# Kernel tuning notes

Measured on AMD Instinct MI355X. Metric: run time of the kernel, lower is better.

Reference implementation:

```python
import jax, jax.numpy as jnp
import numpy as np

SPACE_SIZE = 224
PATCH_SIZE = 16
PATCH_NUM = 196
GRID = SPACE_SIZE // PATCH_SIZE          # 14 patches per axis
OFFSET = 1.0 / (2.0 * GRID)              # half patch width in canonical coords
N_POINTS = 4_000_000


def _pipeline(pc_np):
    """Host-side index pipeline, mirroring the torch module's np.unique usage.
    All outputs are constants w.r.t. differentiation (pure integer indexing)."""
    # voxel quantization: canonical [0,1) -> [0,224); truncation matches torch .long()
    vox = (pc_np * SPACE_SIZE).astype(np.int64)                      # [N,3]
    unq, _, inv = np.unique(vox, return_index=True, return_inverse=True, axis=0)
    inv = inv.reshape(-1)
    num_voxels = unq.shape[0]
    patch = unq // PATCH_SIZE                                        # [U,3]
    # patch_select: keep PATCH_NUM random occupied patches
    p_unq, p_inv = np.unique(patch, return_inverse=True, axis=0)
    p_inv = p_inv.reshape(-1)
    P = p_unq.shape[0]
    sel = np.zeros(P, dtype=bool)
    sel[:PATCH_NUM] = True
    sel = sel[np.random.default_rng(0).permutation(P)]               # randperm mask
    sel_idx = np.nonzero(sel[p_inv])[0]                              # [M] sorted == bool-mask gather
    unq_sel = unq[sel_idx]
    patch_sel = patch[sel_idx]
    patch_unq, patch_unq_indx, patch_unq_inv = np.unique(
        patch_sel, return_index=True, return_inverse=True, axis=0)
    return dict(inv=inv, num_voxels=int(num_voxels), sel_idx=sel_idx,
                unq_sel=unq_sel, patch_sel=patch_sel,
                patch_unq_indx=patch_unq_indx,
                patch_unq_inv=patch_unq_inv.reshape(-1),
                cur_length=int(patch_unq.shape[0]))


def setup_inputs() -> dict:
    key = jax.random.key(0)
    pc_np = np.asarray(jax.random.uniform(key, (N_POINTS, 3), dtype=jnp.float32))
    idx = _pipeline(pc_np)
    return {
        "pc": jnp.asarray(pc_np),
        "inv": jnp.asarray(idx["inv"]),
        "sel_idx": jnp.asarray(idx["sel_idx"]),
        "unq_sel": jnp.asarray(idx["unq_sel"]),
        "patch_sel": jnp.asarray(idx["patch_sel"]),
        "patch_unq_indx": jnp.asarray(idx["patch_unq_indx"]),
        "patch_unq_inv": jnp.asarray(idx["patch_unq_inv"]),
        "num_voxels": idx["num_voxels"],
        "cur_length": idx["cur_length"],
    }


def reference(pc, inv, sel_idx, unq_sel, patch_sel, patch_unq_indx,
              patch_unq_inv, num_voxels, cur_length):
    # scatter-max pooling of point coords into occupied voxels, then select voxels
    features = jax.ops.segment_max(pc, inv, num_segments=num_voxels)[sel_idx]  # [M,3]
    M = features.shape[0]
    # absolute patch coords: patch_indx * 2*offset
    coords_abs = patch_sel.astype(pc.dtype) * (2.0 * OFFSET)                   # [M,3]
    # in-voxel relative hash (x + y*16 + z*256)
    cr = unq_sel % PATCH_SIZE
    coords_rela_query = cr[:, 0] + cr[:, 1] * PATCH_SIZE + cr[:, 2] * PATCH_SIZE ** 2
    # per-patch mean of voxel coords (scatter-mean), gathered back per voxel
    seg_sum = jax.ops.segment_sum(features, patch_unq_inv, num_segments=cur_length)
    seg_cnt = jax.ops.segment_sum(jnp.ones((M, 1), pc.dtype), patch_unq_inv,
                                  num_segments=cur_length)
    voxel_center = (seg_sum / seg_cnt)[patch_unq_inv]                          # [M,3]
    voxel_rela = features - voxel_center
    sel_features = jnp.concatenate([features, voxel_rela, voxel_center], axis=1)  # [M,9]
    # per-selected-patch outputs, padded to PATCH_NUM
    coords_abs_cut = coords_abs[patch_unq_indx]                                # [P,3]
    patch_unq = patch_sel[patch_unq_indx]                                      # [P,3]
    patch_unq_hash = patch_unq[:, 0] + patch_unq[:, 1] * GRID + patch_unq[:, 2] * GRID ** 2
    pad = PATCH_NUM - cur_length
    if pad > 0:
        coords_abs_cut = jnp.concatenate(
            [coords_abs_cut, jnp.zeros((pad, 3), coords_abs_cut.dtype)], axis=0)
        patch_unq_hash = jnp.concatenate(
            [patch_unq_hash, jnp.zeros((pad,), patch_unq_hash.dtype)], axis=0)
    pad_mask = jnp.arange(PATCH_NUM) < cur_length                              # [196]
    r = jnp.arange(PATCH_NUM)
    attn_mask = jnp.where((r[:, None] >= cur_length) & (r[None, :] >= cur_length),
                          -jnp.inf, 0.0).astype(jnp.float32)                   # [196,196]
    # per-voxel (patch id, in-patch 2D coord)
    patch_indicator = jnp.arange(cur_length, dtype=jnp.int32)[patch_unq_inv]   # [M]
    rel = unq_sel - patch_sel * PATCH_SIZE
    sel_coors_inpatch = rel[:, 0:1] * PATCH_SIZE + rel[:, 2:3]
    sel_coors = jnp.concatenate(
        [patch_indicator.reshape(-1, 1).astype(rel.dtype), sel_coors_inpatch], axis=1)
    return (coords_rela_query, coords_abs_cut, sel_coors, sel_features,
            pad_mask, patch_unq_hash, attn_mask)
```

## Files before the change

kernel.cpp:

```cpp
#include <hip/hip_runtime.h>
#include <math.h>

constexpr int TPB = 256;
constexpr int GRIDN = 14;
constexpr int PATCH_NUM = 196;
constexpr int PMAP_N = GRIDN * GRIDN * GRIDN;
constexpr int VPP = 4096;
constexpr int NBS = 1024;
constexpr int TILES = 4;
constexpr int SCAP = 448;
constexpr float QSCALE = 14336.0f;

__device__ __forceinline__ void proc_pt(bool valid, float x, float y, float z,
                                        const unsigned char* __restrict__ spmap,
                                        unsigned* __restrict__ nsel,
                                        unsigned* __restrict__ hist,
                                        unsigned* __restrict__ lrec,
                                        unsigned char* __restrict__ lpid) {
    unsigned s = 255u;
    unsigned rec = 0u;
    if (valid) {
        int ix = (int)(x * QSCALE);
        int iy = (int)(y * QSCALE);
        int iz = (int)(z * QSCALE);
        int pid = ((ix >> 10) * GRIDN + (iy >> 10)) * GRIDN + (iz >> 10);
        s = spmap[pid];
        rec = ((unsigned)(ix & 1023) << 20) | ((unsigned)(iy & 1023) << 10)
            | (unsigned)(iz & 1023);
    }
    bool sel = valid && (s != 255u);
    unsigned long long mask = __ballot(sel);
    if (mask == 0ull) return;
    int lane = threadIdx.x & 63;
    int leader = (int)__ffsll(mask) - 1;
    unsigned base = 0u;
    if (lane == leader) base = atomicAdd(nsel, (unsigned)__popcll(mask));
    base = __shfl(base, leader);
    if (sel) {
        unsigned pos = base + (unsigned)__popcll(mask & ((1ull << lane) - 1ull));
        if (pos < (unsigned)SCAP) {
            lrec[pos] = rec;
            lpid[pos] = (unsigned char)s;
            atomicAdd(&hist[s], 1u);
        }
    }
}

#define LOAD_TILE(T, Q0, Q1, Q2, V0, V1, V2)                       \
    {                                                               \
        int f4b = ((base_pt + (T) * 1024 + wid * 256) * 3) >> 2;    \
        V0 = (f4b + lane) < f4cnt;                                  \
        V1 = (f4b + 64 + lane) < f4cnt;                             \
        V2 = (f4b + 128 + lane) < f4cnt;                            \
        if (V0) Q0 = pc4[f4b + lane];                               \
        if (V1) Q1 = pc4[f4b + 64 + lane];                          \
        if (V2) Q2 = pc4[f4b + 128 + lane];                         \
    }

#define WRITE_STAGE(WS4, Q0, Q1, Q2, V0, V1, V2)                   \
    {                                                               \
        if (V0) (WS4)[lane] = Q0;                                   \
        if (V1) (WS4)[64 + lane] = Q1;                              \
        if (V2) (WS4)[128 + lane] = Q2;                             \
    }

#define PROC_TILE(WS, T)                                                        \
    {                                                                            \
        const float* my = &(WS)[12 * lane];                                      \
        int p0 = base_pt + (T) * 1024 + wid * 256 + lane * 4;                    \
        proc_pt(p0 + 0 < N, my[0], my[1], my[2], spmap, &nsel, hist, lrec, lpid);\
        proc_pt(p0 + 1 < N, my[3], my[4], my[5], spmap, &nsel, hist, lrec, lpid);\
        proc_pt(p0 + 2 < N, my[6], my[7], my[8], spmap, &nsel, hist, lrec, lpid);\
        proc_pt(p0 + 3 < N, my[9], my[10], my[11], spmap, &nsel, hist, lrec, lpid);\
    }

__global__ __launch_bounds__(TPB) void k_main(
        const float* __restrict__ pc, const int* __restrict__ unq_sel,
        const int* __restrict__ puinv, const int* __restrict__ pui,
        const int* __restrict__ psel,
        int* __restrict__ jmap, unsigned* __restrict__ stream,
        unsigned short* __restrict__ offsT,
        float* __restrict__ out, int N, int M, int cur_len, int nbJ,
        int off_crq, int off_sc, int off_attn,
        int off_ca, int off_pm, int off_hash) {
    __shared__ float stage[2][4][768];
    __shared__ unsigned char spmap[PMAP_N];
    __shared__ unsigned hist[256];
    __shared__ unsigned wsum[4];
    __shared__ unsigned cur[256];
    __shared__ unsigned lrec[SCAP];
    __shared__ unsigned char lpid[SCAP];
    __shared__ unsigned sorted_[SCAP];
    __shared__ unsigned nsel;

    int b = blockIdx.x;
    int tid = threadIdx.x;
    if (b < NBS) {
        for (int i = tid; i < PMAP_N; i += TPB) spmap[i] = 255;
        hist[tid] = 0u;
        if (tid == 0) nsel = 0u;
        __syncthreads();
        if (tid < cur_len) {
            int idx = pui[tid];
            spmap[(psel[3 * idx] * GRIDN + psel[3 * idx + 1]) * GRIDN + psel[3 * idx + 2]] =
                (unsigned char)tid;
        }
        __syncthreads();

        const int wid = tid >> 6;
        const int lane = tid & 63;
        const float4* pc4 = (const float4*)pc;
        const int f4cnt = (int)(((long)N * 3) >> 2);
        const int base_pt = b * (TILES * 1024);

        float4 a0, a1, a2, b0, b1, b2;
        bool va0 = false, va1 = false, va2 = false, vb0 = false, vb1 = false, vb2 = false;
        LOAD_TILE(0, a0, a1, a2, va0, va1, va2);
        LOAD_TILE(1, b0, b1, b2, vb0, vb1, vb2);
        #pragma unroll
        for (int t = 0; t < TILES; t += 2) {
            {
                float* ws = stage[0][wid];
                float4* ws4 = (float4*)ws;
                WRITE_STAGE(ws4, a0, a1, a2, va0, va1, va2);
                if (t + 2 < TILES) LOAD_TILE(t + 2, a0, a1, a2, va0, va1, va2);
                PROC_TILE(ws, t);
            }
            {
                float* ws = stage[1][wid];
                float4* ws4 = (float4*)ws;
                WRITE_STAGE(ws4, b0, b1, b2, vb0, vb1, vb2);
                if (t + 3 < TILES) LOAD_TILE(t + 3, b0, b1, b2, vb0, vb1, vb2);
                PROC_TILE(ws, t + 1);
            }
        }
        __syncthreads();

        unsigned v = hist[tid];
        unsigned inc = v;
        for (int d = 1; d < 64; d <<= 1) {
            unsigned o = __shfl_up(inc, d);
            if (lane >= d) inc += o;
        }
        if (lane == 63) wsum[wid] = inc;
        __syncthreads();
        unsigned add = 0;
        for (int w2 = 0; w2 < 4; ++w2) if (w2 < wid) add += wsum[w2];
        unsigned ex = add + inc - v;
        cur[tid] = ex;
        if (tid <= PATCH_NUM)
            offsT[tid * NBS + b] = (unsigned short)ex;
        __syncthreads();

        unsigned ns = nsel;
        if (ns > (unsigned)SCAP) ns = SCAP;
        for (unsigned i = tid; i < ns; i += TPB) {
            unsigned p = lpid[i];
            unsigned d2 = atomicAdd(&cur[p], 1u);
            sorted_[d2] = lrec[i];
        }
        __syncthreads();
        unsigned* sb = stream + (size_t)b * SCAP;
        for (unsigned k = tid; k < ns; k += TPB) sb[k] = sorted_[k];
    } else if (b < NBS + nbJ) {
        int j = (b - NBS) * TPB + tid;
        if (j >= M) return;
        int ux = unq_sel[3 * j + 0];
        int uy = unq_sel[3 * j + 1];
        int uz = unq_sel[3 * j + 2];
        int cx = ux & 15, cy = uy & 15, cz = uz & 15;
        int p = puinv[j];
        jmap[(p << 12) | (cx << 8) | (cy << 4) | cz] = j;
        out[off_crq + j] = (float)(cx + cy * 16 + cz * 256);
        out[off_sc + 2 * j + 0] = (float)p;
        out[off_sc + 2 * j + 1] = (float)(cx * 16 + cz);
    } else {
        int i = (b - NBS - nbJ) * TPB + tid;
        const int nattn = PATCH_NUM * PATCH_NUM;
        if (i < nattn) {
            int r = i / PATCH_NUM;
            int c = i - r * PATCH_NUM;
            out[off_attn + i] = (r >= cur_len && c >= cur_len) ? -INFINITY : 0.0f;
        }
        if (i >= cur_len && i < PATCH_NUM) {
            out[off_ca + 3 * i + 0] = 0.0f;
            out[off_ca + 3 * i + 1] = 0.0f;
            out[off_ca + 3 * i + 2] = 0.0f;
            out[off_hash + i] = 0.0f;
            out[off_pm + i] = 0.0f;
        }
    }
}

__global__ __launch_bounds__(1024) void k_patch_max(
        const unsigned* __restrict__ stream, const unsigned short* __restrict__ offsT,
        const int* __restrict__ pui, const int* __restrict__ psel,
        const int* __restrict__ jmap, float* __restrict__ out,
        int off_sf, int off_ca, int off_pm, int off_hash) {
    __shared__ unsigned gx[VPP];
    __shared__ unsigned gy[VPP];
    __shared__ unsigned gz[VPP];
    __shared__ unsigned occ[VPP / 32];
    __shared__ float wred[4 * 16];
    __shared__ float cc[3];
    int tid = threadIdx.x;
    for (int i = tid; i < VPP; i += 1024) { gx[i] = 0u; gy[i] = 0u; gz[i] = 0u; }
    for (int i = tid; i < VPP / 32; i += 1024) occ[i] = 0u;

    int p = blockIdx.x;
    int idx = pui[p];
    int px = psel[3 * idx + 0];
    int py = psel[3 * idx + 1];
    int pz = psel[3 * idx + 2];

    unsigned o0 = offsT[p * NBS + tid];
    unsigned o1 = offsT[(p + 1) * NBS + tid];
    __syncthreads();

    {
        const unsigned* sp = stream + (size_t)tid * SCAP;
        for (unsigned k = o0; k < o1; ++k) {
            unsigned rec = sp[k];
            unsigned x10 = rec >> 20, y10 = (rec >> 10) & 1023u, z10 = rec & 1023u;
            unsigned v = ((x10 >> 6) << 8) | ((y10 >> 6) << 4) | (z10 >> 6);
            atomicMax(&gx[v], x10 & 63u);
            atomicMax(&gy[v], y10 & 63u);
            atomicMax(&gz[v], z10 & 63u);
            atomicOr(&occ[v >> 5], 1u << (v & 31));
        }
    }
    __syncthreads();

    const float invq = 1.0f / QSCALE;
    float sx = 0.0f, sy = 0.0f, sz = 0.0f;
    int cntv = 0;
    for (int v = tid; v < VPP; v += 1024) {
        if ((occ[v >> 5] >> (v & 31)) & 1u) {
            int gvx = (px << 4) | ((v >> 8) & 15);
            int gvy = (py << 4) | ((v >> 4) & 15);
            int gvz = (pz << 4) | (v & 15);
            sx += (float)((gvx << 6) + (int)gx[v]) * invq;
            sy += (float)((gvy << 6) + (int)gy[v]) * invq;
            sz += (float)((gvz << 6) + (int)gz[v]) * invq;
            cntv++;
        }
    }
    for (int off = 32; off > 0; off >>= 1) {
        sx += __shfl_down(sx, off);
        sy += __shfl_down(sy, off);
        sz += __shfl_down(sz, off);
        cntv += __shfl_down(cntv, off);
    }
    int w = tid >> 6;
    if ((tid & 63) == 0) {
        wred[4 * w + 0] = sx; wred[4 * w + 1] = sy; wred[4 * w + 2] = sz;
        wred[4 * w + 3] = (float)cntv;
    }
    __syncthreads();
    if (tid == 0) {
        float tx = 0.0f, ty = 0.0f, tz = 0.0f, tc = 0.0f;
        for (int i = 0; i < 16; ++i) {
            tx += wred[4 * i]; ty += wred[4 * i + 1]; tz += wred[4 * i + 2]; tc += wred[4 * i + 3];
        }
        cc[0] = tx / tc; cc[1] = ty / tc; cc[2] = tz / tc;
        const float scale = (float)(1.0 / 14.0);
        out[off_ca + 3 * p + 0] = (float)px * scale;
        out[off_ca + 3 * p + 1] = (float)py * scale;
        out[off_ca + 3 * p + 2] = (float)pz * scale;
        out[off_hash + p] = (float)(px + py * GRIDN + pz * GRIDN * GRIDN);
        out[off_pm + p] = 1.0f;
    }
    __syncthreads();

    float ccx = cc[0], ccy = cc[1], ccz = cc[2];
    for (int v = tid; v < VPP; v += 1024) {
        if ((occ[v >> 5] >> (v & 31)) & 1u) {
            int j = jmap[(p << 12) | v];
            int gvx = (px << 4) | ((v >> 8) & 15);
            int gvy = (py << 4) | ((v >> 4) & 15);
            int gvz = (pz << 4) | (v & 15);
            float fx = (float)((gvx << 6) + (int)gx[v]) * invq;
            float fy = (float)((gvy << 6) + (int)gy[v]) * invq;
            float fz = (float)((gvz << 6) + (int)gz[v]) * invq;
            float* sf = &out[off_sf + 9 * (size_t)j];
            sf[0] = fx; sf[1] = fy; sf[2] = fz;
            sf[3] = fx - ccx; sf[4] = fy - ccy; sf[5] = fz - ccz;
            sf[6] = ccx; sf[7] = ccy; sf[8] = ccz;
        }
    }
}


extern "C" void kernel_launch(void* const* d_in, const int* in_sizes, int n_in,
                              void* d_out, int out_size, void* d_ws, size_t ws_size,
                              hipStream_t stream_) {
    const float* pc            = (const float*)d_in[0];
    const int* unq_sel         = (const int*)d_in[3];
    const int* patch_sel       = (const int*)d_in[4];
    const int* patch_unq_indx  = (const int*)d_in[5];
    const int* patch_unq_inv   = (const int*)d_in[6];
    float* out = (float*)d_out;

    const int N = in_sizes[0] / 3;
    const int M = in_sizes[2];
    const int cur_len = in_sizes[5];

    const int off_crq  = 0;
    const int off_ca   = off_crq + M;
    const int off_sc   = off_ca + PATCH_NUM * 3;
    const int off_sf   = off_sc + 2 * M;
    const int off_pm   = off_sf + 9 * M;
    const int off_hash = off_pm + PATCH_NUM;
    const int off_attn = off_hash + PATCH_NUM;

    char* w = (char*)d_ws;
    size_t off = 0;
    unsigned* stream = (unsigned*)(w + off);
    off += (size_t)NBS * SCAP * sizeof(unsigned);
    unsigned short* offsT = (unsigned short*)(w + off);
    off += (size_t)256 * NBS * sizeof(unsigned short);
    off = (off + 255) & ~(size_t)255;
    int* jmap = (int*)(w + off);

    const int nbJ = (M + TPB - 1) / TPB;
    const int nbA = (PATCH_NUM * PATCH_NUM + TPB - 1) / TPB;

    k_main<<<NBS + nbJ + nbA, TPB, 0, stream_>>>(
        pc, unq_sel, patch_unq_inv, patch_unq_indx, patch_sel,
        jmap, stream, offsT, out, N, M, cur_len, nbJ,
        off_crq, off_sc, off_attn, off_ca, off_pm, off_hash);

    k_patch_max<<<cur_len, 1024, 0, stream_>>>(stream, offsT,
                                               patch_unq_indx, patch_sel,
                                               jmap, out, off_sf, off_ca, off_pm, off_hash);
}
```

Measured before the change: 32.30 us.

## Spread point binning over more blocks and alias sort buffer onto staging LDS

The number of binning blocks rises from 1024 to 1280, and the per-block stream capacity drops from 448 to 384. Blocks whose point range starts beyond N now skip the load loop. The sorted buffer reuses the staging shared memory, and the tile loop is rolled into a single register set. The patch kernel now loops over blocks with stride 1024, since 1280 blocks exceed its thread count. This aims to fill more CUs and cut LDS use to raise occupancy, at the cost of a smaller per-block overflow margin and extra serial work for some threads in the patch kernel.

```diff
diff --git a/kernel.cpp b/kernel.cpp
--- a/kernel.cpp
+++ b/kernel.cpp
@@ -6,9 +6,9 @@
 constexpr int PATCH_NUM = 196;
 constexpr int PMAP_N = GRIDN * GRIDN * GRIDN;
 constexpr int VPP = 4096;
-constexpr int NBS = 1024;
+constexpr int NBS = 1280;
 constexpr int TILES = 4;
-constexpr int SCAP = 448;
+constexpr int SCAP = 384;
 constexpr float QSCALE = 14336.0f;
 
 __device__ __forceinline__ void proc_pt(bool valid, float x, float y, float z,
@@ -57,23 +57,6 @@
         if (V2) Q2 = pc4[f4b + 128 + lane];                         \
     }
 
-#define WRITE_STAGE(WS4, Q0, Q1, Q2, V0, V1, V2)                   \
-    {                                                               \
-        if (V0) (WS4)[lane] = Q0;                                   \
-        if (V1) (WS4)[64 + lane] = Q1;                              \
-        if (V2) (WS4)[128 + lane] = Q2;                             \
-    }
-
-#define PROC_TILE(WS, T)                                                        \
-    {                                                                            \
-        const float* my = &(WS)[12 * lane];                                      \
-        int p0 = base_pt + (T) * 1024 + wid * 256 + lane * 4;                    \
-        proc_pt(p0 + 0 < N, my[0], my[1], my[2], spmap, &nsel, hist, lrec, lpid);\
-        proc_pt(p0 + 1 < N, my[3], my[4], my[5], spmap, &nsel, hist, lrec, lpid);\
-        proc_pt(p0 + 2 < N, my[6], my[7], my[8], spmap, &nsel, hist, lrec, lpid);\
-        proc_pt(p0 + 3 < N, my[9], my[10], my[11], spmap, &nsel, hist, lrec, lpid);\
-    }
-
 __global__ __launch_bounds__(TPB) void k_main(
         const float* __restrict__ pc, const int* __restrict__ unq_sel,
         const int* __restrict__ puinv, const int* __restrict__ pui,
@@ -90,12 +73,15 @@
     __shared__ unsigned cur[256];
     __shared__ unsigned lrec[SCAP];
     __shared__ unsigned char lpid[SCAP];
-    __shared__ unsigned sorted_[SCAP];
     __shared__ unsigned nsel;
+    unsigned* sorted_ = (unsigned*)&stage[0][0][0];
 
     int b = blockIdx.x;
     int tid = threadIdx.x;
     if (b < NBS) {
+        const int wid = tid >> 6;
+        const int lane = tid & 63;
+
         for (int i = tid; i < PMAP_N; i += TPB) spmap[i] = 255;
         hist[tid] = 0u;
         if (tid == 0) nsel = 0u;
@@ -107,31 +93,27 @@
         }
         __syncthreads();
 
-        const int wid = tid >> 6;
-        const int lane = tid & 63;
         const float4* pc4 = (const float4*)pc;
         const int f4cnt = (int)(((long)N * 3) >> 2);
         const int base_pt = b * (TILES * 1024);
 
-        float4 a0, a1, a2, b0, b1, b2;
-        bool va0 = false, va1 = false, va2 = false, vb0 = false, vb1 = false, vb2 = false;
-        LOAD_TILE(0, a0, a1, a2, va0, va1, va2);
-        LOAD_TILE(1, b0, b1, b2, vb0, vb1, vb2);
-        #pragma unroll
-        for (int t = 0; t < TILES; t += 2) {
-            {
-                float* ws = stage[0][wid];
+        if (base_pt < N) {
+            float4 q0, q1, q2;
+            bool v0 = false, v1 = false, v2 = false;
+            LOAD_TILE(0, q0, q1, q2, v0, v1, v2);
+            for (int t = 0; t < TILES; ++t) {
+                float* ws = stage[t & 1][wid];
                 float4* ws4 = (float4*)ws;
-                WRITE_STAGE(ws4, a0, a1, a2, va0, va1, va2);
-                if (t + 2 < TILES) LOAD_TILE(t + 2, a0, a1, a2, va0, va1, va2);
-                PROC_TILE(ws, t);
-            }
-            {
-                float* ws = stage[1][wid];
-                float4* ws4 = (float4*)ws;
-                WRITE_STAGE(ws4, b0, b1, b2, vb0, vb1, vb2);
-                if (t + 3 < TILES) LOAD_TILE(t + 3, b0, b1, b2, vb0, vb1, vb2);
-                PROC_TILE(ws, t + 1);
+                if (v0) ws4[lane] = q0;
+                if (v1) ws4[64 + lane] = q1;
+                if (v2) ws4[128 + lane] = q2;
+                if (t + 1 < TILES) LOAD_TILE(t + 1, q0, q1, q2, v0, v1, v2);
+                const float* my = &ws[12 * lane];
+                int p0 = base_pt + t * 1024 + wid * 256 + lane * 4;
+                proc_pt(p0 + 0 < N, my[0], my[1], my[2], spmap, &nsel, hist, lrec, lpid);
+                proc_pt(p0 + 1 < N, my[3], my[4], my[5], spmap, &nsel, hist, lrec, lpid);
+                proc_pt(p0 + 2 < N, my[6], my[7], my[8], spmap, &nsel, hist, lrec, lpid);
+                proc_pt(p0 + 3 < N, my[9], my[10], my[11], spmap, &nsel, hist, lrec, lpid);
             }
         }
         __syncthreads();
@@ -212,13 +194,12 @@
     int px = psel[3 * idx + 0];
     int py = psel[3 * idx + 1];
     int pz = psel[3 * idx + 2];
-
-    unsigned o0 = offsT[p * NBS + tid];
-    unsigned o1 = offsT[(p + 1) * NBS + tid];
     __syncthreads();
 
-    {
-        const unsigned* sp = stream + (size_t)tid * SCAP;
+    for (int b = tid; b < NBS; b += 1024) {
+        unsigned o0 = offsT[p * NBS + b];
+        unsigned o1 = offsT[(p + 1) * NBS + b];
+        const unsigned* sp = stream + (size_t)b * SCAP;
         for (unsigned k = o0; k < o1; ++k) {
             unsigned rec = sp[k];
             unsigned x10 = rec >> 20, y10 = (rec >> 10) & 1023u, z10 = rec & 1023u;
@@ -318,7 +299,7 @@
     unsigned* stream = (unsigned*)(w + off);
     off += (size_t)NBS * SCAP * sizeof(unsigned);
     unsigned short* offsT = (unsigned short*)(w + off);
-    off += (size_t)256 * NBS * sizeof(unsigned short);
+    off += (size_t)(PATCH_NUM + 1) * NBS * sizeof(unsigned short);
     off = (off + 255) & ~(size_t)255;
     int* jmap = (int*)(w + off);
 
```

Measured after the change: 31.22 us. 3.4% less time.
